# Performance work log

Measured on AMD Instinct MI355X. Metric: run time of the kernel, lower is better.

Reference implementation:

```python
import jax, jax.numpy as jnp
import numpy as np

B, T, C = 2, 2048, 1024
R = 16
LORA_SCALE = 1.0 / R  # lora_alpha(=1) / r


def lora_linear(x, w, b, a, bb):
    # loralib: y = x @ W^T + bias + (x @ A^T) @ B^T * scaling
    return x @ w.T + b + (x @ a.T) @ bb.T * LORA_SCALE


def setup_inputs() -> dict:
    key = jax.random.key(0)
    ks = jax.random.split(key, 8)
    s = 0.02
    return {
        "x": jax.random.normal(ks[0], (B, T, C), jnp.float32),
        "w_attn": jax.random.normal(ks[1], (3 * C, C), jnp.float32) * s,
        "b_attn": jnp.zeros((3 * C,), jnp.float32),
        "lora_a_attn": jax.random.normal(ks[2], (R, C), jnp.float32) * s,
        "lora_b_attn": jnp.zeros((3 * C, R), jnp.float32),
        "w_proj": jax.random.normal(ks[3], (C, C), jnp.float32) * s,
        "b_proj": jnp.zeros((C,), jnp.float32),
        "lora_a_proj": jax.random.normal(ks[4], (R, C), jnp.float32) * s,
        "lora_b_proj": jnp.zeros((C, R), jnp.float32),
        "n_head": 16,
    }


def reference(x, w_attn, b_attn, lora_a_attn, lora_b_attn, w_proj, b_proj,
              lora_a_proj, lora_b_proj, n_head):
    b, t, c = x.shape
    hd = c // n_head
    qkv = lora_linear(x, w_attn, b_attn, lora_a_attn, lora_b_attn)
    q, k, v = jnp.split(qkv, 3, axis=2)
    # (B, H, T, hd)
    q = q.reshape(b, t, n_head, hd).transpose(0, 2, 1, 3)
    k = k.reshape(b, t, n_head, hd).transpose(0, 2, 1, 3)
    v = v.reshape(b, t, n_head, hd).transpose(0, 2, 1, 3)
    att = jnp.einsum("bhqd,bhkd->bhqk", q, k) * (1.0 / np.sqrt(hd).astype(np.float32))
    causal = jnp.tril(jnp.ones((t, t), bool))
    att = jnp.where(causal[None, None], att, jnp.float32(-jnp.inf))
    att = jax.nn.softmax(att, axis=-1)
    y = jnp.einsum("bhqk,bhkd->bhqd", att, v)
    y = y.transpose(0, 2, 1, 3).reshape(b, t, c)
    return lora_linear(y, w_proj, b_proj, lora_a_proj, lora_b_proj)
```

## Files before the change

kernel.cpp:

```cpp
#include <hip/hip_runtime.h>

typedef __attribute__((ext_vector_type(8))) short bf16x8;
typedef __attribute__((ext_vector_type(4))) short bf16x4;
typedef __attribute__((ext_vector_type(4))) float f32x4;

__device__ __forceinline__ float bf2f(unsigned short u) {
    unsigned int x = ((unsigned int)u) << 16;
    float f;
    __builtin_memcpy(&f, &x, 4);
    return f;
}
__device__ __forceinline__ unsigned short f2bf(float f) {
    unsigned int x;
    __builtin_memcpy(&x, &f, 4);
    x += 0x7FFFu + ((x >> 16) & 1u);
    return (unsigned short)(x >> 16);
}

#define GLOAD_LDS16(gp, lp)                                      \
    __builtin_amdgcn_global_load_lds(                            \
        (const __attribute__((address_space(1))) void*)(gp),     \
        (__attribute__((address_space(3))) void*)(lp), 16, 0, 0)

__global__ __launch_bounds__(256) void prep(
    const float* __restrict__ x, unsigned short* __restrict__ xb,
    const float* __restrict__ w_attn, const float* __restrict__ la_attn,
    const float* __restrict__ lb_attn, unsigned short* __restrict__ Weff_attn,
    const float* __restrict__ w_proj, const float* __restrict__ la_proj,
    const float* __restrict__ lb_proj, unsigned short* __restrict__ Weff_proj) {
    const int bid = blockIdx.x;
    if (bid < 2048) {
        int i = (bid * 256 + threadIdx.x) * 8;
        float4 v0 = *(const float4*)(x + i);
        float4 v1 = *(const float4*)(x + i + 4);
        bf16x8 o;
        o[0] = (short)f2bf(v0.x); o[1] = (short)f2bf(v0.y);
        o[2] = (short)f2bf(v0.z); o[3] = (short)f2bf(v0.w);
        o[4] = (short)f2bf(v1.x); o[5] = (short)f2bf(v1.y);
        o[6] = (short)f2bf(v1.z); o[7] = (short)f2bf(v1.w);
        *(bf16x8*)(xb + i) = o;
        return;
    }
    const float* W;
    const float* Ain;
    const float* Bin;
    unsigned short* Weff;
    int idx;
    if (bid < 3584) {
        idx = ((bid - 2048) * 256 + threadIdx.x) * 8;
        W = w_attn; Ain = la_attn; Bin = lb_attn; Weff = Weff_attn;
    } else {
        idx = ((bid - 3584) * 256 + threadIdx.x) * 8;
        W = w_proj; Ain = la_proj; Bin = lb_proj; Weff = Weff_proj;
    }
    const int n = idx >> 10;
    const int k = idx & 1023;
    float s[8];
#pragma unroll
    for (int j = 0; j < 8; ++j) s[j] = 0.f;
#pragma unroll
    for (int r = 0; r < 16; ++r) {
        const float bcoef = Bin[n * 16 + r];
        float4 a0 = *(const float4*)(Ain + r * 1024 + k);
        float4 a1 = *(const float4*)(Ain + r * 1024 + k + 4);
        s[0] += bcoef * a0.x; s[1] += bcoef * a0.y;
        s[2] += bcoef * a0.z; s[3] += bcoef * a0.w;
        s[4] += bcoef * a1.x; s[5] += bcoef * a1.y;
        s[6] += bcoef * a1.z; s[7] += bcoef * a1.w;
    }
    float4 w0 = *(const float4*)(W + idx);
    float4 w1 = *(const float4*)(W + idx + 4);
    bf16x8 o;
    o[0] = (short)f2bf(w0.x + 0.0625f * s[0]);
    o[1] = (short)f2bf(w0.y + 0.0625f * s[1]);
    o[2] = (short)f2bf(w0.z + 0.0625f * s[2]);
    o[3] = (short)f2bf(w0.w + 0.0625f * s[3]);
    o[4] = (short)f2bf(w1.x + 0.0625f * s[4]);
    o[5] = (short)f2bf(w1.y + 0.0625f * s[5]);
    o[6] = (short)f2bf(w1.z + 0.0625f * s[6]);
    o[7] = (short)f2bf(w1.w + 0.0625f * s[7]);
    *(bf16x8*)(Weff + idx) = o;
}

template <bool F32OUT, bool VSPLIT>
__global__ __launch_bounds__(256) void gemm_bt_bias(
    const unsigned short* __restrict__ A, const unsigned short* __restrict__ B,
    const float* __restrict__ bias, unsigned short* __restrict__ Cb,
    float* __restrict__ Cf, unsigned short* __restrict__ Vtout,
    int M, int N, int K) {
    __shared__ unsigned short sA0[128 * 32], sA1[128 * 32];
    __shared__ unsigned short sB0[128 * 32], sB1[128 * 32];
    const int tid = threadIdx.x;
    const int wave = tid >> 6, lane = tid & 63;
    const int quad = lane >> 4, l16 = lane & 15;
    const int m0 = blockIdx.y * 128, n0 = blockIdx.x * 128;
    const int wm = (wave & 1) * 64, wn = (wave >> 1) * 64;

    const int srow = wave * 32 + (lane >> 2);
    const int scol = (lane & 3) * 8;
    const unsigned short* Ag = A + (size_t)(m0 + srow) * K + scol;
    const unsigned short* Bg = B + (size_t)(n0 + srow) * K + scol;
    const int woff = wave * 1024;
    const size_t kjump = (size_t)16 * K;

    f32x4 acc[4][4];
#pragma unroll
    for (int i = 0; i < 4; ++i)
#pragma unroll
        for (int j = 0; j < 4; ++j) acc[i][j] = (f32x4){0.f, 0.f, 0.f, 0.f};

    auto stage = [&](unsigned short* dA, unsigned short* dB, int k) {
        GLOAD_LDS16(Ag + k, dA + woff);
        GLOAD_LDS16(Ag + k + kjump, dA + woff + 512);
        GLOAD_LDS16(Bg + k, dB + woff);
        GLOAD_LDS16(Bg + k + kjump, dB + woff + 512);
    };
    auto compute = [&](const unsigned short* cA, const unsigned short* cB) {
        bf16x8 af[4], bfr[4];
#pragma unroll
        for (int mi = 0; mi < 4; ++mi)
            af[mi] = *(const bf16x8*)&cA[(wm + mi * 16 + l16) * 32 + quad * 8];
#pragma unroll
        for (int ni = 0; ni < 4; ++ni)
            bfr[ni] = *(const bf16x8*)&cB[(wn + ni * 16 + l16) * 32 + quad * 8];
#pragma unroll
        for (int mi = 0; mi < 4; ++mi)
#pragma unroll
            for (int ni = 0; ni < 4; ++ni)
                acc[mi][ni] = __builtin_amdgcn_mfma_f32_16x16x32_bf16(
                    af[mi], bfr[ni], acc[mi][ni], 0, 0, 0);
    };

    stage(sA0, sB0, 0);
    __syncthreads();
    for (int k0 = 0; k0 < K; k0 += 64) {
        if (k0 + 32 < K) stage(sA1, sB1, k0 + 32);
        compute(sA0, sB0);
        __syncthreads();
        if (k0 + 64 < K) stage(sA0, sB0, k0 + 64);
        compute(sA1, sB1);
        __syncthreads();
    }

    float bv[4];
#pragma unroll
    for (int ni = 0; ni < 4; ++ni) bv[ni] = bias[n0 + wn + ni * 16 + l16];

    if (VSPLIT && n0 >= 2048) {
#pragma unroll
        for (int ni = 0; ni < 4; ++ni) {
            const int hcol = n0 + wn + ni * 16 + l16 - 2048;
#pragma unroll
            for (int mi = 0; mi < 4; ++mi) {
                const int rowtop = m0 + wm + mi * 16 + quad * 4;
                const int bb = rowtop >> 11;
                const int t = rowtop & 2047;
                bf16x4 pk;
#pragma unroll
                for (int r = 0; r < 4; ++r)
                    pk[r] = (short)f2bf(acc[mi][ni][r] + bv[ni]);
                *(bf16x4*)(Vtout +
                           ((size_t)((bb * 16 + (hcol >> 6)) * 64 + (hcol & 63))) *
                               2048 +
                           t) = pk;
            }
        }
        return;
    }

#pragma unroll
    for (int mi = 0; mi < 4; ++mi)
#pragma unroll
        for (int ni = 0; ni < 4; ++ni)
#pragma unroll
            for (int r = 0; r < 4; ++r) {
                int row = m0 + wm + mi * 16 + quad * 4 + r;
                int col = n0 + wn + ni * 16 + l16;
                float val = acc[mi][ni][r] + bv[ni];
                if (F32OUT)
                    Cf[(size_t)row * N + col] = val;
                else
                    Cb[(size_t)row * N + col] = f2bf(val);
            }
}

__global__ __launch_bounds__(256) void gemm_bt_bias64(
    const unsigned short* __restrict__ A, const unsigned short* __restrict__ B,
    const float* __restrict__ bias, float* __restrict__ Cf,
    int M, int N, int K) {
    __shared__ unsigned short sA0[64 * 32], sA1[64 * 32];
    __shared__ unsigned short sB0[128 * 32], sB1[128 * 32];
    const int tid = threadIdx.x;
    const int wave = tid >> 6, lane = tid & 63;
    const int quad = lane >> 4, l16 = lane & 15;
    const int m0 = blockIdx.y * 64, n0 = blockIdx.x * 128;
    const int wn = wave * 32;

    const int srowA = wave * 16 + (lane >> 2);
    const int srowB = wave * 32 + (lane >> 2);
    const int scol = (lane & 3) * 8;
    const unsigned short* Ag = A + (size_t)(m0 + srowA) * K + scol;
    const unsigned short* Bg = B + (size_t)(n0 + srowB) * K + scol;
    const int woffA = wave * 512, woffB = wave * 1024;
    const size_t kjump = (size_t)16 * K;

    f32x4 acc[4][2];
#pragma unroll
    for (int i = 0; i < 4; ++i)
#pragma unroll
        for (int j = 0; j < 2; ++j) acc[i][j] = (f32x4){0.f, 0.f, 0.f, 0.f};

    auto stage = [&](unsigned short* dA, unsigned short* dB, int k) {
        GLOAD_LDS16(Ag + k, dA + woffA);
        GLOAD_LDS16(Bg + k, dB + woffB);
        GLOAD_LDS16(Bg + k + kjump, dB + woffB + 512);
    };
    auto compute = [&](const unsigned short* cA, const unsigned short* cB) {
        bf16x8 af[4], bfr[2];
#pragma unroll
        for (int mi = 0; mi < 4; ++mi)
            af[mi] = *(const bf16x8*)&cA[(mi * 16 + l16) * 32 + quad * 8];
#pragma unroll
        for (int ni = 0; ni < 2; ++ni)
            bfr[ni] = *(const bf16x8*)&cB[(wn + ni * 16 + l16) * 32 + quad * 8];
#pragma unroll
        for (int mi = 0; mi < 4; ++mi)
#pragma unroll
            for (int ni = 0; ni < 2; ++ni)
                acc[mi][ni] = __builtin_amdgcn_mfma_f32_16x16x32_bf16(
                    af[mi], bfr[ni], acc[mi][ni], 0, 0, 0);
    };

    stage(sA0, sB0, 0);
    __syncthreads();
    for (int k0 = 0; k0 < K; k0 += 64) {
        if (k0 + 32 < K) stage(sA1, sB1, k0 + 32);
        compute(sA0, sB0);
        __syncthreads();
        if (k0 + 64 < K) stage(sA0, sB0, k0 + 64);
        compute(sA1, sB1);
        __syncthreads();
    }

    float bv[2];
#pragma unroll
    for (int ni = 0; ni < 2; ++ni) bv[ni] = bias[n0 + wn + ni * 16 + l16];
#pragma unroll
    for (int mi = 0; mi < 4; ++mi)
#pragma unroll
        for (int ni = 0; ni < 2; ++ni)
#pragma unroll
            for (int r = 0; r < 4; ++r) {
                int row = m0 + mi * 16 + quad * 4 + r;
                int col = n0 + wn + ni * 16 + l16;
                Cf[(size_t)row * N + col] = acc[mi][ni][r] + bv[ni];
            }
}

__global__ __launch_bounds__(256, 4) void attn_kernel(
    const unsigned short* __restrict__ qkv,
    const unsigned short* __restrict__ Vt,
    unsigned short* __restrict__ y) {
    const int b = blockIdx.z, h = blockIdx.y;
    const int bh = b * 16 + h;
    const int qblk = (int)blockIdx.x ^ (((bh >> 3) & 1) ? 31 : 0);
    const int w = threadIdx.x >> 6, lane = threadIdx.x & 63;
    const int quad = lane >> 4, l16 = lane & 15;
    const int qh = w & 1, kvh = w >> 1;
    const int q0 = qblk * 64 + qh * 32;
    const int ntiles = qblk + 1;

    __shared__ __align__(16) char smem[2 * 18432 + 512];
    unsigned short* bufA = (unsigned short*)smem;
    unsigned short* bufB = (unsigned short*)(smem + 18432);
    float* sO = (float*)smem;
    float* sD = (float*)(smem + 2 * 18432);

    const unsigned short* Qb = qkv + (size_t)(b * 2048) * 3072 + h * 64;
    const unsigned short* Kg = Qb + 1024;
    const unsigned short* Vg = Vt + (size_t)(bh * 64) * 2048;

    const int rlo = threadIdx.x >> 3;
    const int c8 = (threadIdx.x & 7) * 8;

    bf16x8 qf[2][2];
#pragma unroll
    for (int m = 0; m < 2; ++m) {
        qf[m][0] = *(const bf16x8*)(Qb + (size_t)(q0 + m * 16 + l16) * 3072 + quad * 8);
        qf[m][1] = *(const bf16x8*)(Qb + (size_t)(q0 + m * 16 + l16) * 3072 + 32 + quad * 8);
    }

    const int krow0 = kvh * 32 + 8 * (l16 >> 2) + (l16 & 3);

    f32x4 o[2][4];
    float lacc[2] = {0.f, 0.f};
#pragma unroll
    for (int m = 0; m < 2; ++m)
#pragma unroll
        for (int nt = 0; nt < 4; ++nt) o[m][nt] = (f32x4){0.f, 0.f, 0.f, 0.f};

    const float csc = 0.125f * 1.44269504088896340736f;

    bf16x8 kr0 = *(const bf16x8*)(Kg + (size_t)rlo * 3072 + c8);
    bf16x8 kr1 = *(const bf16x8*)(Kg + (size_t)(rlo + 32) * 3072 + c8);
    bf16x8 vr0 = *(const bf16x8*)(Vg + (size_t)rlo * 2048 + c8);
    bf16x8 vr1 = *(const bf16x8*)(Vg + (size_t)(rlo + 32) * 2048 + c8);
    {
        unsigned short* sK = bufA;
        unsigned short* sV = bufA + 64 * 72;
        *(bf16x8*)&sK[rlo * 72 + c8] = kr0;
        *(bf16x8*)&sK[(rlo + 32) * 72 + c8] = kr1;
        *(bf16x8*)&sV[rlo * 72 + c8] = vr0;
        *(bf16x8*)&sV[(rlo + 32) * 72 + c8] = vr1;
    }
    __syncthreads();

    unsigned short* bcur = bufA;
    unsigned short* bnxt = bufB;

    for (int it = 0; it < ntiles; ++it) {
        const bool pf = (it + 1 < ntiles);
        if (pf) {
            const int nx = (it + 1) * 64;
            kr0 = *(const bf16x8*)(Kg + (size_t)(nx + rlo) * 3072 + c8);
            kr1 = *(const bf16x8*)(Kg + (size_t)(nx + rlo + 32) * 3072 + c8);
            vr0 = *(const bf16x8*)(Vg + (size_t)rlo * 2048 + nx + c8);
            vr1 = *(const bf16x8*)(Vg + (size_t)(rlo + 32) * 2048 + nx + c8);
        }

        const unsigned short* sK = bcur;
        const unsigned short* sV = bcur + 64 * 72;

        bf16x8 ka[2][2];
#pragma unroll
        for (int f = 0; f < 2; ++f) {
            ka[f][0] = *(const bf16x8*)&sK[(krow0 + 4 * f) * 72 + quad * 8];
            ka[f][1] = *(const bf16x8*)&sK[(krow0 + 4 * f) * 72 + 32 + quad * 8];
        }
        bf16x8 vb[4];
#pragma unroll
        for (int nt = 0; nt < 4; ++nt)
            vb[nt] = *(const bf16x8*)&sV[(nt * 16 + l16) * 72 + kvh * 32 + quad * 8];

        const int kv0 = it * 64;
        const bool diag = (it == qblk);
#pragma unroll
        for (int m = 0; m < 2; ++m) {
            const int qa = q0 + m * 16 + l16;
            unsigned int pw[4];
            float lsum = 0.f;
#pragma unroll
            for (int f = 0; f < 2; ++f) {
                f32x4 S = (f32x4){0.f, 0.f, 0.f, 0.f};
                S = __builtin_amdgcn_mfma_f32_16x16x32_bf16(ka[f][0], qf[m][0], S, 0, 0, 0);
                S = __builtin_amdgcn_mfma_f32_16x16x32_bf16(ka[f][1], qf[m][1], S, 0, 0, 0);
                float p0, p1, p2, p3;
                {
                    float sv = S[0] * csc;
                    asm("v_exp_f32 %0, %1" : "=v"(p0) : "v"(sv));
                    sv = S[1] * csc;
                    asm("v_exp_f32 %0, %1" : "=v"(p1) : "v"(sv));
                    sv = S[2] * csc;
                    asm("v_exp_f32 %0, %1" : "=v"(p2) : "v"(sv));
                    sv = S[3] * csc;
                    asm("v_exp_f32 %0, %1" : "=v"(p3) : "v"(sv));
                }
                if (diag) {
                    int kvb = kv0 + kvh * 32 + 8 * quad + 4 * f;
                    p0 = (kvb + 0 <= qa) ? p0 : 0.f;
                    p1 = (kvb + 1 <= qa) ? p1 : 0.f;
                    p2 = (kvb + 2 <= qa) ? p2 : 0.f;
                    p3 = (kvb + 3 <= qa) ? p3 : 0.f;
                }
                lsum += (p0 + p1) + (p2 + p3);
                asm("v_cvt_pk_bf16_f32 %0, %1, %2" : "=v"(pw[f * 2 + 0]) : "v"(p0), "v"(p1));
                asm("v_cvt_pk_bf16_f32 %0, %1, %2" : "=v"(pw[f * 2 + 1]) : "v"(p2), "v"(p3));
            }
            lacc[m] += lsum;
            union {
                unsigned int u[4];
                bf16x8 v;
            } pa;
            pa.u[0] = pw[0]; pa.u[1] = pw[1]; pa.u[2] = pw[2]; pa.u[3] = pw[3];
#pragma unroll
            for (int nt = 0; nt < 4; ++nt)
                o[m][nt] = __builtin_amdgcn_mfma_f32_16x16x32_bf16(
                    pa.v, vb[nt], o[m][nt], 0, 0, 0);
        }

        if (pf) {
            unsigned short* dK = bnxt;
            unsigned short* dV = bnxt + 64 * 72;
            *(bf16x8*)&dK[rlo * 72 + c8] = kr0;
            *(bf16x8*)&dK[(rlo + 32) * 72 + c8] = kr1;
            *(bf16x8*)&dV[rlo * 72 + c8] = vr0;
            *(bf16x8*)&dV[(rlo + 32) * 72 + c8] = vr1;
        }
        __syncthreads();
        unsigned short* t = bcur; bcur = bnxt; bnxt = t;
    }

#pragma unroll
    for (int m = 0; m < 2; ++m) {
        lacc[m] += __shfl_xor(lacc[m], 16);
        lacc[m] += __shfl_xor(lacc[m], 32);
    }

    if (kvh == 1) {
        float* dst = sO + qh * (64 * 36);
#pragma unroll
        for (int m = 0; m < 2; ++m)
#pragma unroll
            for (int nt = 0; nt < 4; ++nt)
                *(f32x4*)&dst[(nt * 16 + l16) * 36 + m * 16 + quad * 4] = o[m][nt];
    }
    if (lane < 16) {
        sD[w * 32 + l16] = lacc[0];
        sD[w * 32 + 16 + l16] = lacc[1];
    }
    __syncthreads();
    if (kvh == 0) {
        const float* src = sO + qh * (64 * 36);
        unsigned short* yb = y + (size_t)(b * 2048) * 1024 + h * 64;
#pragma unroll
        for (int m = 0; m < 2; ++m) {
            float dfull = lacc[m] + sD[(w + 2) * 32 + m * 16 + l16];
            float lt[4];
#pragma unroll
            for (int r = 0; r < 4; ++r) lt[r] = __shfl(dfull, quad * 4 + r);
#pragma unroll
            for (int nt = 0; nt < 4; ++nt) {
                f32x4 part = *(const f32x4*)&src[(nt * 16 + l16) * 36 + m * 16 + quad * 4];
#pragma unroll
                for (int r = 0; r < 4; ++r)
                    yb[(size_t)(q0 + m * 16 + quad * 4 + r) * 1024 + nt * 16 + l16] =
                        f2bf((o[m][nt][r] + part[r]) / lt[r]);
            }
        }
    }
}

extern "C" void kernel_launch(void* const* d_in, const int* in_sizes, int n_in,
                              void* d_out, int out_size, void* d_ws, size_t ws_size,
                              hipStream_t stream) {
    const float* x       = (const float*)d_in[0];
    const float* w_attn  = (const float*)d_in[1];
    const float* b_attn  = (const float*)d_in[2];
    const float* la_attn = (const float*)d_in[3];
    const float* lb_attn = (const float*)d_in[4];
    const float* w_proj  = (const float*)d_in[5];
    const float* b_proj  = (const float*)d_in[6];
    const float* la_proj = (const float*)d_in[7];
    const float* lb_proj = (const float*)d_in[8];
    float* out = (float*)d_out;

    char* w = (char*)d_ws;
    unsigned short* xb        = (unsigned short*)w; w += (size_t)4096 * 1024 * 2;
    unsigned short* Weff_attn = (unsigned short*)w; w += (size_t)3072 * 1024 * 2;
    unsigned short* Weff_proj = (unsigned short*)w; w += (size_t)1024 * 1024 * 2;
    unsigned short* qkv       = (unsigned short*)w; w += (size_t)4096 * 3072 * 2;
    unsigned short* Vt        = (unsigned short*)w; w += (size_t)32 * 64 * 2048 * 2;
    unsigned short* y         = (unsigned short*)w; w += (size_t)4096 * 1024 * 2;

    prep<<<4096, 256, 0, stream>>>(x, xb, w_attn, la_attn, lb_attn, Weff_attn,
                                   w_proj, la_proj, lb_proj, Weff_proj);
    gemm_bt_bias<false, true><<<dim3(24, 32), 256, 0, stream>>>(
        xb, Weff_attn, b_attn, qkv, (float*)nullptr, Vt, 4096, 3072, 1024);
    attn_kernel<<<dim3(32, 16, 2), 256, 0, stream>>>(qkv, Vt, y);
    gemm_bt_bias64<<<dim3(8, 64), 256, 0, stream>>>(
        y, Weff_proj, b_proj, out, 4096, 1024, 1024);
}
```

Measured before the change: 187.9 us.

## Halve attention query tile to 32 rows, double grid, heaviest-first ordering

The attention kernel now gives each block 32 query rows (16 per wave) instead of 64, doubling the grid to 64 blocks per head and launching the longest causal tiles first via a reversed block index. This replaces the old XOR pairing for load balance and adds s_setprio around the PV MFMAs. The intent is more parallelism and a smaller causal tail. In exchange each K/V tile loaded into LDS is reused by half as many queries, so LDS and global traffic per unit of work roughly doubles.

```diff
diff --git a/kernel.cpp b/kernel.cpp
--- a/kernel.cpp
+++ b/kernel.cpp
@@ -263,12 +263,12 @@
     unsigned short* __restrict__ y) {
     const int b = blockIdx.z, h = blockIdx.y;
     const int bh = b * 16 + h;
-    const int qblk = (int)blockIdx.x ^ (((bh >> 3) & 1) ? 31 : 0);
+    const int j = 63 - (int)blockIdx.x;
     const int w = threadIdx.x >> 6, lane = threadIdx.x & 63;
     const int quad = lane >> 4, l16 = lane & 15;
     const int qh = w & 1, kvh = w >> 1;
-    const int q0 = qblk * 64 + qh * 32;
-    const int ntiles = qblk + 1;
+    const int q0 = j * 32 + qh * 16;
+    const int ntiles = (j >> 1) + 1;
 
     __shared__ __align__(16) char smem[2 * 18432 + 512];
     unsigned short* bufA = (unsigned short*)smem;
@@ -283,21 +283,15 @@
     const int rlo = threadIdx.x >> 3;
     const int c8 = (threadIdx.x & 7) * 8;
 
-    bf16x8 qf[2][2];
-#pragma unroll
-    for (int m = 0; m < 2; ++m) {
-        qf[m][0] = *(const bf16x8*)(Qb + (size_t)(q0 + m * 16 + l16) * 3072 + quad * 8);
-        qf[m][1] = *(const bf16x8*)(Qb + (size_t)(q0 + m * 16 + l16) * 3072 + 32 + quad * 8);
-    }
+    bf16x8 qf0 = *(const bf16x8*)(Qb + (size_t)(q0 + l16) * 3072 + quad * 8);
+    bf16x8 qf1 = *(const bf16x8*)(Qb + (size_t)(q0 + l16) * 3072 + 32 + quad * 8);
 
     const int krow0 = kvh * 32 + 8 * (l16 >> 2) + (l16 & 3);
 
-    f32x4 o[2][4];
-    float lacc[2] = {0.f, 0.f};
-#pragma unroll
-    for (int m = 0; m < 2; ++m)
-#pragma unroll
-        for (int nt = 0; nt < 4; ++nt) o[m][nt] = (f32x4){0.f, 0.f, 0.f, 0.f};
+    f32x4 o[4];
+    float lacc = 0.f;
+#pragma unroll
+    for (int nt = 0; nt < 4; ++nt) o[nt] = (f32x4){0.f, 0.f, 0.f, 0.f};
 
     const float csc = 0.125f * 1.44269504088896340736f;
 
@@ -343,50 +337,49 @@
             vb[nt] = *(const bf16x8*)&sV[(nt * 16 + l16) * 72 + kvh * 32 + quad * 8];
 
         const int kv0 = it * 64;
-        const bool diag = (it == qblk);
-#pragma unroll
-        for (int m = 0; m < 2; ++m) {
-            const int qa = q0 + m * 16 + l16;
-            unsigned int pw[4];
-            float lsum = 0.f;
-#pragma unroll
-            for (int f = 0; f < 2; ++f) {
-                f32x4 S = (f32x4){0.f, 0.f, 0.f, 0.f};
-                S = __builtin_amdgcn_mfma_f32_16x16x32_bf16(ka[f][0], qf[m][0], S, 0, 0, 0);
-                S = __builtin_amdgcn_mfma_f32_16x16x32_bf16(ka[f][1], qf[m][1], S, 0, 0, 0);
-                float p0, p1, p2, p3;
-                {
-                    float sv = S[0] * csc;
-                    asm("v_exp_f32 %0, %1" : "=v"(p0) : "v"(sv));
-                    sv = S[1] * csc;
-                    asm("v_exp_f32 %0, %1" : "=v"(p1) : "v"(sv));
-                    sv = S[2] * csc;
-                    asm("v_exp_f32 %0, %1" : "=v"(p2) : "v"(sv));
-                    sv = S[3] * csc;
-                    asm("v_exp_f32 %0, %1" : "=v"(p3) : "v"(sv));
-                }
-                if (diag) {
-                    int kvb = kv0 + kvh * 32 + 8 * quad + 4 * f;
-                    p0 = (kvb + 0 <= qa) ? p0 : 0.f;
-                    p1 = (kvb + 1 <= qa) ? p1 : 0.f;
-                    p2 = (kvb + 2 <= qa) ? p2 : 0.f;
-                    p3 = (kvb + 3 <= qa) ? p3 : 0.f;
-                }
-                lsum += (p0 + p1) + (p2 + p3);
-                asm("v_cvt_pk_bf16_f32 %0, %1, %2" : "=v"(pw[f * 2 + 0]) : "v"(p0), "v"(p1));
-                asm("v_cvt_pk_bf16_f32 %0, %1, %2" : "=v"(pw[f * 2 + 1]) : "v"(p2), "v"(p3));
+        const bool diag = (it == ntiles - 1);
+        const int qa = q0 + l16;
+        unsigned int pw[4];
+        float lsum = 0.f;
+#pragma unroll
+        for (int f = 0; f < 2; ++f) {
+            f32x4 S = (f32x4){0.f, 0.f, 0.f, 0.f};
+            S = __builtin_amdgcn_mfma_f32_16x16x32_bf16(ka[f][0], qf0, S, 0, 0, 0);
+            S = __builtin_amdgcn_mfma_f32_16x16x32_bf16(ka[f][1], qf1, S, 0, 0, 0);
+            float p0, p1, p2, p3;
+            {
+                float sv = S[0] * csc;
+                asm("v_exp_f32 %0, %1" : "=v"(p0) : "v"(sv));
+                sv = S[1] * csc;
+                asm("v_exp_f32 %0, %1" : "=v"(p1) : "v"(sv));
+                sv = S[2] * csc;
+                asm("v_exp_f32 %0, %1" : "=v"(p2) : "v"(sv));
+                sv = S[3] * csc;
+                asm("v_exp_f32 %0, %1" : "=v"(p3) : "v"(sv));
             }
-            lacc[m] += lsum;
-            union {
-                unsigned int u[4];
-                bf16x8 v;
-            } pa;
-            pa.u[0] = pw[0]; pa.u[1] = pw[1]; pa.u[2] = pw[2]; pa.u[3] = pw[3];
-#pragma unroll
-            for (int nt = 0; nt < 4; ++nt)
-                o[m][nt] = __builtin_amdgcn_mfma_f32_16x16x32_bf16(
-                    pa.v, vb[nt], o[m][nt], 0, 0, 0);
-        }
+            if (diag) {
+                int kvb = kv0 + kvh * 32 + 8 * quad + 4 * f;
+                p0 = (kvb + 0 <= qa) ? p0 : 0.f;
+                p1 = (kvb + 1 <= qa) ? p1 : 0.f;
+                p2 = (kvb + 2 <= qa) ? p2 : 0.f;
+                p3 = (kvb + 3 <= qa) ? p3 : 0.f;
+            }
+            lsum += (p0 + p1) + (p2 + p3);
+            asm("v_cvt_pk_bf16_f32 %0, %1, %2" : "=v"(pw[f * 2 + 0]) : "v"(p0), "v"(p1));
+            asm("v_cvt_pk_bf16_f32 %0, %1, %2" : "=v"(pw[f * 2 + 1]) : "v"(p2), "v"(p3));
+        }
+        lacc += lsum;
+        union {
+            unsigned int u[4];
+            bf16x8 v;
+        } pa;
+        pa.u[0] = pw[0]; pa.u[1] = pw[1]; pa.u[2] = pw[2]; pa.u[3] = pw[3];
+        __builtin_amdgcn_s_setprio(1);
+#pragma unroll
+        for (int nt = 0; nt < 4; ++nt)
+            o[nt] = __builtin_amdgcn_mfma_f32_16x16x32_bf16(
+                pa.v, vb[nt], o[nt], 0, 0, 0);
+        __builtin_amdgcn_s_setprio(0);
 
         if (pf) {
             unsigned short* dK = bnxt;
@@ -400,42 +393,31 @@
         unsigned short* t = bcur; bcur = bnxt; bnxt = t;
     }
 
-#pragma unroll
-    for (int m = 0; m < 2; ++m) {
-        lacc[m] += __shfl_xor(lacc[m], 16);
-        lacc[m] += __shfl_xor(lacc[m], 32);
-    }
+    lacc += __shfl_xor(lacc, 16);
+    lacc += __shfl_xor(lacc, 32);
 
     if (kvh == 1) {
-        float* dst = sO + qh * (64 * 36);
-#pragma unroll
-        for (int m = 0; m < 2; ++m)
-#pragma unroll
-            for (int nt = 0; nt < 4; ++nt)
-                *(f32x4*)&dst[(nt * 16 + l16) * 36 + m * 16 + quad * 4] = o[m][nt];
-    }
-    if (lane < 16) {
-        sD[w * 32 + l16] = lacc[0];
-        sD[w * 32 + 16 + l16] = lacc[1];
-    }
+        float* dst = sO + qh * (64 * 20);
+#pragma unroll
+        for (int nt = 0; nt < 4; ++nt)
+            *(f32x4*)&dst[(nt * 16 + l16) * 20 + quad * 4] = o[nt];
+    }
+    if (lane < 16) sD[w * 16 + l16] = lacc;
     __syncthreads();
     if (kvh == 0) {
-        const float* src = sO + qh * (64 * 36);
+        const float* src = sO + qh * (64 * 20);
         unsigned short* yb = y + (size_t)(b * 2048) * 1024 + h * 64;
-#pragma unroll
-        for (int m = 0; m < 2; ++m) {
-            float dfull = lacc[m] + sD[(w + 2) * 32 + m * 16 + l16];
-            float lt[4];
-#pragma unroll
-            for (int r = 0; r < 4; ++r) lt[r] = __shfl(dfull, quad * 4 + r);
-#pragma unroll
-            for (int nt = 0; nt < 4; ++nt) {
-                f32x4 part = *(const f32x4*)&src[(nt * 16 + l16) * 36 + m * 16 + quad * 4];
-#pragma unroll
-                for (int r = 0; r < 4; ++r)
-                    yb[(size_t)(q0 + m * 16 + quad * 4 + r) * 1024 + nt * 16 + l16] =
-                        f2bf((o[m][nt][r] + part[r]) / lt[r]);
-            }
+        float dfull = lacc + sD[(w + 2) * 16 + l16];
+        float lt[4];
+#pragma unroll
+        for (int r = 0; r < 4; ++r) lt[r] = __shfl(dfull, quad * 4 + r);
+#pragma unroll
+        for (int nt = 0; nt < 4; ++nt) {
+            f32x4 part = *(const f32x4*)&src[(nt * 16 + l16) * 20 + quad * 4];
+#pragma unroll
+            for (int r = 0; r < 4; ++r)
+                yb[(size_t)(q0 + quad * 4 + r) * 1024 + nt * 16 + l16] =
+                    f2bf((o[nt][r] + part[r]) / lt[r]);
         }
     }
 }
@@ -466,7 +448,7 @@
                                    w_proj, la_proj, lb_proj, Weff_proj);
     gemm_bt_bias<false, true><<<dim3(24, 32), 256, 0, stream>>>(
         xb, Weff_attn, b_attn, qkv, (float*)nullptr, Vt, 4096, 3072, 1024);
-    attn_kernel<<<dim3(32, 16, 2), 256, 0, stream>>>(qkv, Vt, y);
+    attn_kernel<<<dim3(64, 16, 2), 256, 0, stream>>>(qkv, Vt, y);
     gemm_bt_bias64<<<dim3(8, 64), 256, 0, stream>>>(
         y, Weff_proj, b_proj, out, 4096, 1024, 1024);
 }
```

Result: slower. 212.3 us (+13.0%).
